# Kernel tuning notes

Hardware: AMD Instinct MI355X
Metric: run time of the kernel (lower is better)

## Reference

```python
import jax, jax.numpy as jnp
import numpy as np

# Complete binary tree: node 0 is the root, node i's parent is (i-1)//2.
# adjacency[i, j] = 1 iff j is the parent of i (matches _parent_indices/_child_indices).
N_LEVELS = 11
N_LABELS = 2 ** N_LEVELS - 1  # 2047
N_CLASSES = 2
BATCH = 2048


def _tree_structure():
    # levels[t]: node ids at tree level t (root level 0)
    levels = [np.arange(2 ** t - 1, 2 ** (t + 1) - 1) for t in range(N_LEVELS)]
    parent = np.zeros(N_LABELS, dtype=np.int64)
    parent[1:] = (np.arange(1, N_LABELS) - 1) // 2
    return levels, parent


def _propagate(emissions, transitions, edge_layers):
    """Belief-propagation sweep. edge_layers is a list (per depth, in order)
    of (src, dst) numpy index arrays: each src node sends a message to dst.
    Message: m[b, c_dst, dst] += logsumexp_{c_src}(emissions[b,c_src,src]
              + messages[b,c_src,src] + transitions[dst, src, c_dst, c_src]).
    Identical math to (Batched)MessagePassing.forward, expressed per edge.
    """
    messages = jnp.zeros_like(emissions)
    for src, dst in edge_layers:
        e = emissions[:, :, src] + messages[:, :, src]           # [B, Cs, E]
        t = transitions[dst, src]                                 # [E, Cd, Cs]
        # elem[b, cd, e, cs] = e[b, cs, e] + t[e, cd, cs]
        elem = e.transpose(0, 2, 1)[:, None, :, :] + t.transpose(1, 0, 2)[None]
        contrib = jax.nn.logsumexp(elem, axis=-1)                 # [B, Cd, E]
        messages = messages.at[:, :, dst].add(contrib)
    return messages


def setup_inputs() -> dict:
    key = jax.random.key(0)
    k1, k2 = jax.random.split(key)
    emissions = jax.random.normal(k1, (BATCH, N_CLASSES, N_LABELS), dtype=jnp.float32)
    transitions = jax.random.normal(k2, (N_LABELS, N_LABELS, N_CLASSES, N_CLASSES), dtype=jnp.float32)
    return {"emissions": emissions, "transitions": transitions}


def reference(emissions, transitions):
    levels, parent = _tree_structure()
    # upward (alphas): leaves -> root, successor = parent
    up_edges = [(levels[t], parent[levels[t]]) for t in range(N_LEVELS - 1, 0, -1)]
    # downward (betas): root -> leaves, successor = child
    down_edges = [(parent[levels[t]], levels[t]) for t in range(1, N_LEVELS)]
    alphas = _propagate(emissions, transitions, up_edges)
    betas = _propagate(emissions, transitions, down_edges)
    scores = emissions + alphas + betas                           # [B, C, L]
    # normalize over classes per label -> marginal log-probabilities
    return scores - jax.nn.logsumexp(scores, axis=1, keepdims=True)
```

## Files before the change

### kernel.cpp

```cpp
#include <hip/hip_runtime.h>


#define N_LEVELS 11
#define N_LABELS 2047
#define BATCH    2048
#define NTHREADS 256

__device__ __forceinline__ float lse2(float x, float y) {
    float m = fmaxf(x, y);
    float d = fminf(x, y) - m;
    return m + __logf(1.0f + __expf(d));
}

__global__ __launch_bounds__(NTHREADS) void treecrf_kernel(
    const float* __restrict__ emissions,
    const float* __restrict__ transitions,
    float* __restrict__ out)
{
    __shared__ float em[2 * N_LABELS];
    __shared__ float alphas[2 * N_LABELS];
    __shared__ float betas[2 * N_LABELS];

    const int b = blockIdx.x;
    const int tid = threadIdx.x;
    const float* emg = emissions + (size_t)b * (2 * N_LABELS);
    float* outg = out + (size_t)b * (2 * N_LABELS);
    const float4* tr4 = (const float4*)transitions;

    {
        const float2* src = (const float2*)emg;
        float2* dst = (float2*)em;
        for (int i = tid; i < N_LABELS; i += NTHREADS) dst[i] = src[i];
    }
    for (int i = tid; i < 1024; i += NTHREADS) {
        alphas[1023 + i] = 0.f;
        alphas[N_LABELS + 1023 + i] = 0.f;
    }
    __syncthreads();

    for (int lvl = N_LEVELS - 2; lvl >= 0; --lvl) {
        const int base = (1 << lvl) - 1;
        const int n = 1 << lvl;
        for (int off = tid; off < n; off += NTHREADS) {
            const int p = base + off;
            const int c0 = 2 * p + 1, c1 = c0 + 1;
            const float a00 = em[c0] + alphas[c0];
            const float a01 = em[N_LABELS + c0] + alphas[N_LABELS + c0];
            const float a10 = em[c1] + alphas[c1];
            const float a11 = em[N_LABELS + c1] + alphas[N_LABELS + c1];
            const float4 t0 = tr4[p * N_LABELS + c0];
            const float4 t1 = tr4[p * N_LABELS + c1];
            alphas[p]            = lse2(a00 + t0.x, a01 + t0.y)
                                 + lse2(a10 + t1.x, a11 + t1.y);
            alphas[N_LABELS + p] = lse2(a00 + t0.z, a01 + t0.w)
                                 + lse2(a10 + t1.z, a11 + t1.w);
        }
        __syncthreads();
    }

    if (tid == 0) {
        betas[0] = 0.f; betas[N_LABELS] = 0.f;
        const float s0 = em[0] + alphas[0];
        const float s1 = em[N_LABELS] + alphas[N_LABELS];
        const float l = lse2(s0, s1);
        outg[0] = s0 - l;
        outg[N_LABELS] = s1 - l;
    }
    __syncthreads();

    for (int lvl = 1; lvl < N_LEVELS; ++lvl) {
        const int base = (1 << lvl) - 1;
        const int n = 1 << lvl;
        for (int off = tid; off < n; off += NTHREADS) {
            const int i = base + off;
            const int p = (i - 1) >> 1;
            const float b0 = em[p] + betas[p];
            const float b1 = em[N_LABELS + p] + betas[N_LABELS + p];
            const float4 t = tr4[i * N_LABELS + p];
            const float v0 = lse2(b0 + t.x, b1 + t.y);
            const float v1 = lse2(b0 + t.z, b1 + t.w);
            betas[i] = v0;
            betas[N_LABELS + i] = v1;
            const float s0 = em[i] + alphas[i] + v0;
            const float s1 = em[N_LABELS + i] + alphas[N_LABELS + i] + v1;
            const float l = lse2(s0, s1);
            outg[i] = s0 - l;
            outg[N_LABELS + i] = s1 - l;
        }
        __syncthreads();
    }
}

extern "C" void kernel_launch(void* const* d_in, const int* in_sizes, int n_in,
                              void* d_out, int out_size, void* d_ws, size_t ws_size,
                              hipStream_t stream) {
    const float* emissions   = (const float*)d_in[0];
    const float* transitions = (const float*)d_in[1];
    float* out = (float*)d_out;
    treecrf_kernel<<<BATCH, NTHREADS, 0, stream>>>(emissions, transitions, out);
}
```

Before: 161.8 us.

## Prefetch all transition entries into registers and fold emissions into shared arrays

```diff
diff --git a/kernel.cpp b/kernel.cpp
--- a/kernel.cpp
+++ b/kernel.cpp
@@ -1,10 +1,8 @@
 #include <hip/hip_runtime.h>
 
 
-#define N_LEVELS 11
-#define N_LABELS 2047
-#define BATCH    2048
-#define NTHREADS 256
+#define L  2047
+#define NT 256
 
 __device__ __forceinline__ float lse2(float x, float y) {
     float m = fmaxf(x, y);
@@ -12,83 +10,152 @@
     return m + __logf(1.0f + __expf(d));
 }
 
-__global__ __launch_bounds__(NTHREADS) void treecrf_kernel(
+#define UP_NODE(p, ta, tb) do {                                             \
+    const int _c0 = 2*(p) + 1;                                              \
+    const float _a00 = A[_c0],     _a01 = A[L + _c0];                       \
+    const float _a10 = A[_c0 + 1], _a11 = A[L + _c0 + 1];                   \
+    const float _al0 = lse2(_a00 + (ta).x, _a01 + (ta).y)                   \
+                     + lse2(_a10 + (tb).x, _a11 + (tb).y);                  \
+    const float _al1 = lse2(_a00 + (ta).z, _a01 + (ta).w)                   \
+                     + lse2(_a10 + (tb).z, _a11 + (tb).w);                  \
+    A[(p)]     = em[(p)]     + _al0;                                        \
+    A[L + (p)] = em[L + (p)] + _al1;                                        \
+} while (0)
+
+#define DN_NODE(i, t, WRITE_EM) do {                                        \
+    const int _p = ((i) - 1) >> 1;                                          \
+    const float _b0 = em[_p], _b1 = em[L + _p];                             \
+    const float _v0 = lse2(_b0 + (t).x, _b1 + (t).y);                       \
+    const float _v1 = lse2(_b0 + (t).z, _b1 + (t).w);                       \
+    if (WRITE_EM) { em[(i)] += _v0; em[L + (i)] += _v1; }                   \
+    const float _s0 = A[(i)] + _v0, _s1 = A[L + (i)] + _v1;                 \
+    const float _l = lse2(_s0, _s1);                                        \
+    outg[(i)] = _s0 - _l; outg[L + (i)] = _s1 - _l;                         \
+} while (0)
+
+__global__ __launch_bounds__(NT) void treecrf_kernel(
     const float* __restrict__ emissions,
     const float* __restrict__ transitions,
     float* __restrict__ out)
 {
-    __shared__ float em[2 * N_LABELS];
-    __shared__ float alphas[2 * N_LABELS];
-    __shared__ float betas[2 * N_LABELS];
+    __shared__ float em[2 * L];
+    __shared__ float A[2 * L];
 
     const int b = blockIdx.x;
     const int tid = threadIdx.x;
-    const float* emg = emissions + (size_t)b * (2 * N_LABELS);
-    float* outg = out + (size_t)b * (2 * N_LABELS);
-    const float4* tr4 = (const float4*)transitions;
+    const float* __restrict__ emg = emissions + (size_t)b * (2 * L);
+    float* __restrict__ outg = out + (size_t)b * (2 * L);
+    const float4* __restrict__ tr4 = (const float4*)transitions;
+
+    int up_p = 0, dn_i = 1;
+    if (tid < 128)      { up_p = 127 + tid;         dn_i = 127 + tid; }
+    else if (tid < 192) { up_p = 63 + (tid - 128);  dn_i = 63 + (tid - 128); }
+    else if (tid < 224) { up_p = 31 + (tid - 192);  dn_i = 31 + (tid - 192); }
+    else if (tid < 240) { up_p = 15 + (tid - 224);  dn_i = 15 + (tid - 224); }
+    else if (tid < 248) { up_p = 7 + (tid - 240);   dn_i = 7 + (tid - 240); }
+    else if (tid < 252) { up_p = 3 + (tid - 248);   dn_i = 3 + (tid - 248); }
+    else if (tid < 254) { up_p = 1 + (tid - 252);   dn_i = 1 + (tid - 252); }
+
+    float4 u9a0, u9a1, u9b0, u9b1, u8a, u8b, usa, usb;
+    {
+        int p = 511 + tid;
+        const float4* q = tr4 + p * L + (2 * p + 1);
+        u9a0 = q[0]; u9a1 = q[1];
+        p = 767 + tid;
+        q = tr4 + p * L + (2 * p + 1);
+        u9b0 = q[0]; u9b1 = q[1];
+        p = 255 + tid;
+        q = tr4 + p * L + (2 * p + 1);
+        u8a = q[0]; u8b = q[1];
+        p = up_p;
+        q = tr4 + p * L + (2 * p + 1);
+        usa = q[0]; usb = q[1];
+    }
 
     {
-        const float2* src = (const float2*)emg;
+        const float2* __restrict__ src = (const float2*)emg;
         float2* dst = (float2*)em;
-        for (int i = tid; i < N_LABELS; i += NTHREADS) dst[i] = src[i];
+        #pragma unroll
+        for (int k = 0; k < 8; ++k) {
+            int i = tid + k * NT;
+            if (i < L) dst[i] = src[i];
+        }
     }
-    for (int i = tid; i < 1024; i += NTHREADS) {
-        alphas[1023 + i] = 0.f;
-        alphas[N_LABELS + 1023 + i] = 0.f;
+    #pragma unroll
+    for (int k = 0; k < 4; ++k) {
+        int i = tid + k * NT;
+        A[1023 + i]     = emg[1023 + i];
+        A[L + 1023 + i] = emg[L + 1023 + i];
     }
     __syncthreads();
 
-    for (int lvl = N_LEVELS - 2; lvl >= 0; --lvl) {
-        const int base = (1 << lvl) - 1;
-        const int n = 1 << lvl;
-        for (int off = tid; off < n; off += NTHREADS) {
-            const int p = base + off;
-            const int c0 = 2 * p + 1, c1 = c0 + 1;
-            const float a00 = em[c0] + alphas[c0];
-            const float a01 = em[N_LABELS + c0] + alphas[N_LABELS + c0];
-            const float a10 = em[c1] + alphas[c1];
-            const float a11 = em[N_LABELS + c1] + alphas[N_LABELS + c1];
-            const float4 t0 = tr4[p * N_LABELS + c0];
-            const float4 t1 = tr4[p * N_LABELS + c1];
-            alphas[p]            = lse2(a00 + t0.x, a01 + t0.y)
-                                 + lse2(a10 + t1.x, a11 + t1.y);
-            alphas[N_LABELS + p] = lse2(a00 + t0.z, a01 + t0.w)
-                                 + lse2(a10 + t1.z, a11 + t1.w);
-        }
-        __syncthreads();
-    }
+    UP_NODE(511 + tid, u9a0, u9a1);
+    UP_NODE(767 + tid, u9b0, u9b1);
 
-    if (tid == 0) {
-        betas[0] = 0.f; betas[N_LABELS] = 0.f;
-        const float s0 = em[0] + alphas[0];
-        const float s1 = em[N_LABELS] + alphas[N_LABELS];
-        const float l = lse2(s0, s1);
-        outg[0] = s0 - l;
-        outg[N_LABELS] = s1 - l;
+    float4 d10a, d10b, d10c, d10d, d9a, d9b, d8, ds;
+    {
+        int i = 1023 + tid;        d10a = tr4[i * L + ((i - 1) >> 1)];
+        i = 1279 + tid;            d10b = tr4[i * L + ((i - 1) >> 1)];
+        i = 1535 + tid;            d10c = tr4[i * L + ((i - 1) >> 1)];
+        i = 1791 + tid;            d10d = tr4[i * L + ((i - 1) >> 1)];
+        i = 511 + tid;             d9a  = tr4[i * L + ((i - 1) >> 1)];
+        i = 767 + tid;             d9b  = tr4[i * L + ((i - 1) >> 1)];
+        i = 255 + tid;             d8   = tr4[i * L + ((i - 1) >> 1)];
+        i = dn_i;                  ds   = tr4[i * L + ((i - 1) >> 1)];
     }
     __syncthreads();
 
-    for (int lvl = 1; lvl < N_LEVELS; ++lvl) {
-        const int base = (1 << lvl) - 1;
-        const int n = 1 << lvl;
-        for (int off = tid; off < n; off += NTHREADS) {
-            const int i = base + off;
-            const int p = (i - 1) >> 1;
-            const float b0 = em[p] + betas[p];
-            const float b1 = em[N_LABELS + p] + betas[N_LABELS + p];
-            const float4 t = tr4[i * N_LABELS + p];
-            const float v0 = lse2(b0 + t.x, b1 + t.y);
-            const float v1 = lse2(b0 + t.z, b1 + t.w);
-            betas[i] = v0;
-            betas[N_LABELS + i] = v1;
-            const float s0 = em[i] + alphas[i] + v0;
-            const float s1 = em[N_LABELS + i] + alphas[N_LABELS + i] + v1;
-            const float l = lse2(s0, s1);
-            outg[i] = s0 - l;
-            outg[N_LABELS + i] = s1 - l;
-        }
-        __syncthreads();
+    UP_NODE(255 + tid, u8a, u8b);
+    __syncthreads();
+
+    if (tid < 128)                 UP_NODE(up_p, usa, usb);
+    __syncthreads();
+    if (tid >= 128 && tid < 192)   UP_NODE(up_p, usa, usb);
+    __syncthreads();
+    if (tid >= 192 && tid < 224)   UP_NODE(up_p, usa, usb);
+    __syncthreads();
+    if (tid >= 224 && tid < 240)   UP_NODE(up_p, usa, usb);
+    __syncthreads();
+    if (tid >= 240 && tid < 248)   UP_NODE(up_p, usa, usb);
+    __syncthreads();
+    if (tid >= 248 && tid < 252)   UP_NODE(up_p, usa, usb);
+    __syncthreads();
+    if (tid >= 252 && tid < 254)   UP_NODE(up_p, usa, usb);
+    __syncthreads();
+
+    if (tid == 254)                UP_NODE(0, usa, usb);
+    if (tid >= 252 && tid < 254)   DN_NODE(dn_i, ds, 1);
+    __syncthreads();
+
+    if (tid == 255) {
+        const float s0 = A[0], s1 = A[L];
+        const float l = lse2(s0, s1);
+        outg[0] = s0 - l; outg[L] = s1 - l;
     }
+    if (tid >= 248 && tid < 252)   DN_NODE(dn_i, ds, 1);
+    __syncthreads();
+    if (tid >= 240 && tid < 248)   DN_NODE(dn_i, ds, 1);
+    __syncthreads();
+    if (tid >= 224 && tid < 240)   DN_NODE(dn_i, ds, 1);
+    __syncthreads();
+    if (tid >= 192 && tid < 224)   DN_NODE(dn_i, ds, 1);
+    __syncthreads();
+    if (tid >= 128 && tid < 192)   DN_NODE(dn_i, ds, 1);
+    __syncthreads();
+    if (tid < 128)                 DN_NODE(dn_i, ds, 1);
+    __syncthreads();
+
+    DN_NODE(255 + tid, d8, 1);
+    __syncthreads();
+
+    DN_NODE(511 + tid, d9a, 1);
+    DN_NODE(767 + tid, d9b, 1);
+    __syncthreads();
+
+    DN_NODE(1023 + tid, d10a, 0);
+    DN_NODE(1279 + tid, d10b, 0);
+    DN_NODE(1535 + tid, d10c, 0);
+    DN_NODE(1791 + tid, d10d, 0);
 }
 
 extern "C" void kernel_launch(void* const* d_in, const int* in_sizes, int n_in,
@@ -97,5 +164,5 @@
     const float* emissions   = (const float*)d_in[0];
     const float* transitions = (const float*)d_in[1];
     float* out = (float*)d_out;
-    treecrf_kernel<<<BATCH, NTHREADS, 0, stream>>>(emissions, transitions, out);
+    treecrf_kernel<<<2048, NT, 0, stream>>>(emissions, transitions, out);
 }
```

Measured after the change: 154.5 us. 4.5% less time.
